# Kernel optimization log

Measured on AMD Instinct MI355X. Metric: run time of the kernel, lower is better.

Reference implementation:

```python
import jax, jax.numpy as jnp
import numpy as np

H1, H2 = 96, 64


def _lstm_scan(x_tbd, Wih, Whh, bih, bhh, hidden):
    """x_tbd: [T, B, D]. Returns (outputs [T, B, hidden], final h [B, hidden]).
    PyTorch gate order: i, f, g, o."""
    T, B, _ = x_tbd.shape
    b = bih + bhh  # fuse biases once
    # precompute input projections for all timesteps: [T, B, 4H]
    x_proj = jnp.einsum('tbd,hd->tbh', x_tbd, Wih) + b

    def step(carry, xp):
        h, c = carry
        gates = xp + h @ Whh.T  # [B, 4H]
        i, f, g, o = jnp.split(gates, 4, axis=-1)
        i = jax.nn.sigmoid(i)
        f = jax.nn.sigmoid(f)
        g = jnp.tanh(g)
        o = jax.nn.sigmoid(o)
        c = f * c + i * g
        h = o * jnp.tanh(c)
        return (h, c), h

    h0 = jnp.zeros((B, hidden), x_tbd.dtype)
    c0 = jnp.zeros((B, hidden), x_tbd.dtype)
    (hT, _), hs = jax.lax.scan(step, (h0, c0), x_proj)
    return hs, hT


def setup_inputs() -> dict:
    key = jax.random.key(0)
    ks = jax.random.split(key, 16)
    B, T, D, HOR = 4096, 336, 8, 24
    s1 = 1.0 / np.sqrt(H1)
    s2 = 1.0 / np.sqrt(H2)
    u = lambda k, shape, s: jax.random.uniform(k, shape, jnp.float32, -s, s)
    return {
        'x': jax.random.normal(ks[0], (B, T, D), jnp.float32),
        'Wih1': u(ks[1], (4 * H1, D), s1),
        'Whh1': u(ks[2], (4 * H1, H1), s1),
        'bih1': u(ks[3], (4 * H1,), s1),
        'bhh1': u(ks[4], (4 * H1,), s1),
        'Wih2': u(ks[5], (4 * H2, H1), s2),
        'Whh2': u(ks[6], (4 * H2, H2), s2),
        'bih2': u(ks[7], (4 * H2,), s2),
        'bhh2': u(ks[8], (4 * H2,), s2),
        'fc1_w': u(ks[9], (64, H2), s2),
        'fc1_b': u(ks[10], (64,), s2),
        'fco_w': u(ks[11], (HOR, 64), s2),
        'fco_b': u(ks[12], (HOR,), s2),
    }


def reference(x, Wih1, Whh1, bih1, bhh1, Wih2, Whh2, bih2, bhh2,
              fc1_w, fc1_b, fco_w, fco_b):
    # dropout layers are identity in eval mode
    x_tbd = jnp.transpose(x, (1, 0, 2))  # [T, B, D]
    hs1, _ = _lstm_scan(x_tbd, Wih1, Whh1, bih1, bhh1, H1)  # [T, B, 96]
    _, hT2 = _lstm_scan(hs1, Wih2, Whh2, bih2, bhh2, H2)    # [B, 64] = last timestep
    h = jax.nn.relu(hT2 @ fc1_w.T + fc1_b)
    return h @ fco_w.T + fco_b  # [B, horizon]
```

## Files before the change

kernel.cpp:

```cpp
#include <hip/hip_runtime.h>
#include <hip/hip_bf16.h>

namespace {

constexpr int T_LEN = 336;
constexpr int D_IN  = 8;
constexpr int NH1   = 96;
constexpr int NH2   = 64;
constexpr int HOR   = 24;
constexpr int BM    = 16;
constexpr int KPAD  = 200;


typedef __attribute__((ext_vector_type(8))) short short8;
typedef __attribute__((ext_vector_type(4))) float f32x4;

__device__ inline unsigned short f2b(float f) {
  union { float f; unsigned u; } v; v.f = f;
  unsigned r = v.u + 0x7fffu + ((v.u >> 16) & 1u);
  return (unsigned short)(r >> 16);
}

__device__ inline short8 pack8(float4 p0, float4 p1) {
  short8 f;
  f[0]=(short)f2b(p0.x); f[1]=(short)f2b(p0.y); f[2]=(short)f2b(p0.z); f[3]=(short)f2b(p0.w);
  f[4]=(short)f2b(p1.x); f[5]=(short)f2b(p1.y); f[6]=(short)f2b(p1.z); f[7]=(short)f2b(p1.w);
  return f;
}

__device__ inline float sigf(float x)   { return __builtin_amdgcn_rcpf(1.0f + __expf(-x)); }
__device__ inline float tanhf_(float x) { return 1.0f - 2.0f * __builtin_amdgcn_rcpf(1.0f + __expf(2.0f * x)); }

__global__ __launch_bounds__(512, 2) void lstm_forecaster(
    const float* __restrict__ x,
    const float* __restrict__ Wih1, const float* __restrict__ Whh1,
    const float* __restrict__ bih1, const float* __restrict__ bhh1,
    const float* __restrict__ Wih2, const float* __restrict__ Whh2,
    const float* __restrict__ bih2, const float* __restrict__ bhh2,
    const float* __restrict__ fc1w, const float* __restrict__ fc1b,
    const float* __restrict__ fcow, const float* __restrict__ fcob,
    float* __restrict__ out)
{
  __shared__ unsigned short Hc[2][BM * KPAD];
  __shared__ float h2f[BM][NH2];
  __shared__ float fcb[BM][NH2 + 4];

  const int tid  = threadIdx.x;
  const int w    = tid >> 6;
  const int l    = tid & 63;
  const int lrow = l & 15;
  const int lgrp = l >> 4;
  const int b0   = blockIdx.x * BM;

  const float* xrow = x + (size_t)(b0 + lrow) * (T_LEN * D_IN) + lgrp * 2;
  float2 xv = make_float2(0.0f, 0.0f);
  if (w == 0) xv = *(const float2*)(xrow);

  for (int i = tid; i < 2 * BM * KPAD; i += 512) ((unsigned short*)Hc)[i] = 0;

  short8 a1[3][4];
  #pragma unroll
  for (int mt = 0; mt < 3; ++mt) {
    const int gate = lrow & 3;
    const int cell = w * 12 + mt * 4 + (lrow >> 2);
    const int wrow = NH1 * gate + cell;
    #pragma unroll
    for (int kt = 0; kt < 4; ++kt) {
      const int kb = kt * 32 + lgrp * 8;
      if (kb < NH1) {
        a1[mt][kt] = pack8(*(const float4*)(Whh1 + wrow * NH1 + kb),
                           *(const float4*)(Whh1 + wrow * NH1 + kb + 4));
      } else if (kb == NH1) {
        a1[mt][kt] = pack8(*(const float4*)(Wih1 + wrow * D_IN),
                           *(const float4*)(Wih1 + wrow * D_IN + 4));
      } else {
        short8 z;
        #pragma unroll
        for (int e = 0; e < 8; ++e) z[e] = 0;
        a1[mt][kt] = z;
      }
    }
  }
  short8 a2[2][5];
  #pragma unroll
  for (int mt = 0; mt < 2; ++mt) {
    const int gate = lrow & 3;
    const int cell = w * 8 + mt * 4 + (lrow >> 2);
    const int wrow = NH2 * gate + cell;
    #pragma unroll
    for (int kt = 0; kt < 5; ++kt) {
      const int kb = kt * 32 + lgrp * 8;
      if (kb < NH2) {
        a2[mt][kt] = pack8(*(const float4*)(Whh2 + wrow * NH2 + kb),
                           *(const float4*)(Whh2 + wrow * NH2 + kb + 4));
      } else {
        a2[mt][kt] = pack8(*(const float4*)(Wih2 + wrow * NH1 + (kb - NH2)),
                           *(const float4*)(Wih2 + wrow * NH1 + (kb - NH2) + 4));
      }
    }
  }

  float bias1[3][4], bias2[2][4];
  #pragma unroll
  for (int mt = 0; mt < 3; ++mt) {
    const int cell = w * 12 + mt * 4 + lgrp;
    #pragma unroll
    for (int r = 0; r < 4; ++r)
      bias1[mt][r] = bih1[NH1 * r + cell] + bhh1[NH1 * r + cell];
  }
  #pragma unroll
  for (int mt = 0; mt < 2; ++mt) {
    const int cell = w * 8 + mt * 4 + lgrp;
    #pragma unroll
    for (int r = 0; r < 4; ++r)
      bias2[mt][r] = bih2[NH2 * r + cell] + bhh2[NH2 * r + cell];
  }

  __syncthreads();
  if (w == 0) {
    unsigned p = (unsigned)f2b(xv.x) | ((unsigned)f2b(xv.y) << 16);
    *(unsigned*)&Hc[1][lrow * KPAD + 160 + lgrp * 2] = p;
  }
  __syncthreads();

  float c1[3] = {0.0f, 0.0f, 0.0f};
  float c2[2] = {0.0f, 0.0f};
  const int rbo = lrow * KPAD;

  {
    if (w == 0) xv = *(const float2*)(xrow + D_IN);
    short8 b1[4];
    #pragma unroll
    for (int kt = 0; kt < 4; ++kt)
      b1[kt] = *(const short8*)(&Hc[1][rbo + 64 + lgrp * 8 + kt * 32]);
    #pragma unroll
    for (int mt = 0; mt < 3; ++mt) {
      f32x4 acc = { bias1[mt][0], bias1[mt][1], bias1[mt][2], bias1[mt][3] };
      #pragma unroll
      for (int kt = 0; kt < 4; ++kt)
        acc = __builtin_amdgcn_mfma_f32_16x16x32_bf16(a1[mt][kt], b1[kt], acc, 0, 0, 0);
      const float ig = sigf(acc[0]), fg = sigf(acc[1]);
      const float gg = tanhf_(acc[2]), og = sigf(acc[3]);
      c1[mt] = fg * c1[mt] + ig * gg;
      Hc[0][rbo + 64 + w * 12 + mt * 4 + lgrp] = f2b(og * tanhf_(c1[mt]));
    }
    if (w == 0) {
      unsigned p = (unsigned)f2b(xv.x) | ((unsigned)f2b(xv.y) << 16);
      *(unsigned*)&Hc[0][lrow * KPAD + 160 + lgrp * 2] = p;
    }
    __syncthreads();
  }

  for (int p = 0; p < T_LEN - 1; ++p) {
    const unsigned short* RB = &Hc[p & 1][0];
    unsigned short*       WB = &Hc[(p & 1) ^ 1][0];

    if (w == 0 && p + 2 < T_LEN)
      xv = *(const float2*)(xrow + (p + 2) * D_IN);

    short8 b2[5], b1[4];
    #pragma unroll
    for (int kt = 0; kt < 5; ++kt)
      b2[kt] = *(const short8*)(RB + rbo + lgrp * 8 + kt * 32);
    #pragma unroll
    for (int kt = 0; kt < 4; ++kt)
      b1[kt] = *(const short8*)(RB + rbo + 64 + lgrp * 8 + kt * 32);

    f32x4 acc2[2];
    #pragma unroll
    for (int mt = 0; mt < 2; ++mt) {
      acc2[mt] = f32x4{ bias2[mt][0], bias2[mt][1], bias2[mt][2], bias2[mt][3] };
      #pragma unroll
      for (int kt = 0; kt < 5; ++kt)
        acc2[mt] = __builtin_amdgcn_mfma_f32_16x16x32_bf16(a2[mt][kt], b2[kt], acc2[mt], 0, 0, 0);
    }
    f32x4 acc1[3];
    #pragma unroll
    for (int mt = 0; mt < 3; ++mt) {
      acc1[mt] = f32x4{ bias1[mt][0], bias1[mt][1], bias1[mt][2], bias1[mt][3] };
      #pragma unroll
      for (int kt = 0; kt < 4; ++kt)
        acc1[mt] = __builtin_amdgcn_mfma_f32_16x16x32_bf16(a1[mt][kt], b1[kt], acc1[mt], 0, 0, 0);
    }

    #pragma unroll
    for (int mt = 0; mt < 2; ++mt) {
      const float ig = sigf(acc2[mt][0]), fg = sigf(acc2[mt][1]);
      const float gg = tanhf_(acc2[mt][2]), og = sigf(acc2[mt][3]);
      c2[mt] = fg * c2[mt] + ig * gg;
      WB[rbo + w * 8 + mt * 4 + lgrp] = f2b(og * tanhf_(c2[mt]));
    }
    #pragma unroll
    for (int mt = 0; mt < 3; ++mt) {
      const float ig = sigf(acc1[mt][0]), fg = sigf(acc1[mt][1]);
      const float gg = tanhf_(acc1[mt][2]), og = sigf(acc1[mt][3]);
      c1[mt] = fg * c1[mt] + ig * gg;
      WB[rbo + 64 + w * 12 + mt * 4 + lgrp] = f2b(og * tanhf_(c1[mt]));
    }
    if (w == 0 && p + 2 < T_LEN) {
      unsigned pk = (unsigned)f2b(xv.x) | ((unsigned)f2b(xv.y) << 16);
      *(unsigned*)&WB[lrow * KPAD + 160 + lgrp * 2] = pk;
    }
    __syncthreads();
  }

  {
    const unsigned short* RB = &Hc[(T_LEN - 1) & 1][0];
    short8 b2[5];
    #pragma unroll
    for (int kt = 0; kt < 5; ++kt)
      b2[kt] = *(const short8*)(RB + rbo + lgrp * 8 + kt * 32);
    #pragma unroll
    for (int mt = 0; mt < 2; ++mt) {
      f32x4 acc = { bias2[mt][0], bias2[mt][1], bias2[mt][2], bias2[mt][3] };
      #pragma unroll
      for (int kt = 0; kt < 5; ++kt)
        acc = __builtin_amdgcn_mfma_f32_16x16x32_bf16(a2[mt][kt], b2[kt], acc, 0, 0, 0);
      const float ig = sigf(acc[0]), fg = sigf(acc[1]);
      const float gg = tanhf_(acc[2]), og = sigf(acc[3]);
      const float cf = fg * c2[mt] + ig * gg;
      h2f[lrow][w * 8 + mt * 4 + lgrp] = og * tanhf_(cf);
    }
  }
  __syncthreads();

  for (int p = tid; p < BM * NH2; p += 512) {
    const int col = p >> 6;
    const int j   = p & 63;
    float s = fc1b[j];
    const float* wr = fc1w + j * NH2;
    #pragma unroll 8
    for (int k = 0; k < NH2; ++k) s += h2f[col][k] * wr[k];
    fcb[col][j] = fmaxf(s, 0.0f);
  }
  __syncthreads();
  if (tid < BM * HOR) {
    const int col = tid / HOR;
    const int oc  = tid - col * HOR;
    float s = fcob[oc];
    const float* wr = fcow + oc * NH2;
    #pragma unroll 8
    for (int k = 0; k < NH2; ++k) s += fcb[col][k] * wr[k];
    out[(size_t)(b0 + col) * HOR + oc] = s;
  }
}

}

extern "C" void kernel_launch(void* const* d_in, const int* in_sizes, int n_in,
                              void* d_out, int out_size, void* d_ws, size_t ws_size,
                              hipStream_t stream) {
  const float* x    = (const float*)d_in[0];
  const float* Wih1 = (const float*)d_in[1];
  const float* Whh1 = (const float*)d_in[2];
  const float* bih1 = (const float*)d_in[3];
  const float* bhh1 = (const float*)d_in[4];
  const float* Wih2 = (const float*)d_in[5];
  const float* Whh2 = (const float*)d_in[6];
  const float* bih2 = (const float*)d_in[7];
  const float* bhh2 = (const float*)d_in[8];
  const float* fc1w = (const float*)d_in[9];
  const float* fc1b = (const float*)d_in[10];
  const float* fcow = (const float*)d_in[11];
  const float* fcob = (const float*)d_in[12];
  float* out = (float*)d_out;

  const int Btot = in_sizes[0] / (T_LEN * D_IN);
  const int nblk = Btot / BM;

  lstm_forecaster<<<dim3(nblk), dim3(512), 0, stream>>>(
      x, Wih1, Whh1, bih1, bhh1, Wih2, Whh2, bih2, bhh2,
      fc1w, fc1b, fcow, fcob, out);
}
```

Before: 361.6 us.

## Split layer-1 and layer-2 LSTM work across separate wave groups

The block grows from 512 to 1024 threads. Waves 0-7 now compute only layer 1 and waves 8-15 compute only layer 2, where before every wave computed both layers. Each wave holds about half as many weight fragments in registers, and the two layers' MFMA and activation chains run concurrently on different waves. Float-to-bf16 conversion also switches to the packed v_cvt_pk_bf16_f32 instruction. The risks are that the 1024-thread block with launch bounds of 4 blocks per CU squeezes the register budget, and that the per-step barrier now spans twice as many waves.

Measured after the change: 343.5 us. 5.0% less time.

```diff
diff --git a/kernel.cpp b/kernel.cpp
--- a/kernel.cpp
+++ b/kernel.cpp
@@ -28,10 +28,16 @@
   return f;
 }
 
+__device__ inline unsigned cvt_pk_bf16(float a, float b) {
+  unsigned r;
+  asm("v_cvt_pk_bf16_f32 %0, %1, %2" : "=v"(r) : "v"(a), "v"(b));
+  return r;
+}
+
 __device__ inline float sigf(float x)   { return __builtin_amdgcn_rcpf(1.0f + __expf(-x)); }
 __device__ inline float tanhf_(float x) { return 1.0f - 2.0f * __builtin_amdgcn_rcpf(1.0f + __expf(2.0f * x)); }
 
-__global__ __launch_bounds__(512, 2) void lstm_forecaster(
+__global__ __launch_bounds__(1024, 4) void lstm_forecaster(
     const float* __restrict__ x,
     const float* __restrict__ Wih1, const float* __restrict__ Whh1,
     const float* __restrict__ bih1, const float* __restrict__ bhh1,
@@ -51,102 +57,98 @@
   const int lrow = l & 15;
   const int lgrp = l >> 4;
   const int b0   = blockIdx.x * BM;
+  const bool isL1 = (w < 8);
+  const int  wv   = isL1 ? w : (w - 8);
 
   const float* xrow = x + (size_t)(b0 + lrow) * (T_LEN * D_IN) + lgrp * 2;
   float2 xv = make_float2(0.0f, 0.0f);
-  if (w == 0) xv = *(const float2*)(xrow);
-
-  for (int i = tid; i < 2 * BM * KPAD; i += 512) ((unsigned short*)Hc)[i] = 0;
-
-  short8 a1[3][4];
-  #pragma unroll
-  for (int mt = 0; mt < 3; ++mt) {
-    const int gate = lrow & 3;
-    const int cell = w * 12 + mt * 4 + (lrow >> 2);
-    const int wrow = NH1 * gate + cell;
-    #pragma unroll
-    for (int kt = 0; kt < 4; ++kt) {
-      const int kb = kt * 32 + lgrp * 8;
-      if (kb < NH1) {
-        a1[mt][kt] = pack8(*(const float4*)(Whh1 + wrow * NH1 + kb),
-                           *(const float4*)(Whh1 + wrow * NH1 + kb + 4));
-      } else if (kb == NH1) {
-        a1[mt][kt] = pack8(*(const float4*)(Wih1 + wrow * D_IN),
-                           *(const float4*)(Wih1 + wrow * D_IN + 4));
-      } else {
-        short8 z;
+  if (w == 8) xv = *(const float2*)(xrow);
+
+  for (int i = tid; i < 2 * BM * KPAD; i += 1024) ((unsigned short*)Hc)[i] = 0;
+
+  short8 af[12];
+  float  bs[12];
+  if (isL1) {
+    #pragma unroll
+    for (int mt = 0; mt < 3; ++mt) {
+      const int gate = lrow & 3;
+      const int cell = wv * 12 + mt * 4 + (lrow >> 2);
+      const int wrow = NH1 * gate + cell;
+      #pragma unroll
+      for (int kt = 0; kt < 4; ++kt) {
+        const int kb = kt * 32 + lgrp * 8;
+        if (kb < NH1) {
+          af[mt*4+kt] = pack8(*(const float4*)(Whh1 + wrow * NH1 + kb),
+                              *(const float4*)(Whh1 + wrow * NH1 + kb + 4));
+        } else if (kb == NH1) {
+          af[mt*4+kt] = pack8(*(const float4*)(Wih1 + wrow * D_IN),
+                              *(const float4*)(Wih1 + wrow * D_IN + 4));
+        } else {
+          short8 z;
+          #pragma unroll
+          for (int e = 0; e < 8; ++e) z[e] = 0;
+          af[mt*4+kt] = z;
+        }
+      }
+      const int bcell = wv * 12 + mt * 4 + lgrp;
+      #pragma unroll
+      for (int r = 0; r < 4; ++r)
+        bs[mt*4+r] = bih1[NH1 * r + bcell] + bhh1[NH1 * r + bcell];
+    }
+  } else {
+    #pragma unroll
+    for (int mt = 0; mt < 2; ++mt) {
+      const int gate = lrow & 3;
+      const int cell = wv * 8 + mt * 4 + (lrow >> 2);
+      const int wrow = NH2 * gate + cell;
+      #pragma unroll
+      for (int kt = 0; kt < 5; ++kt) {
+        const int kb = kt * 32 + lgrp * 8;
+        if (kb < NH2) {
+          af[mt*5+kt] = pack8(*(const float4*)(Whh2 + wrow * NH2 + kb),
+                              *(const float4*)(Whh2 + wrow * NH2 + kb + 4));
+        } else {
+          af[mt*5+kt] = pack8(*(const float4*)(Wih2 + wrow * NH1 + (kb - NH2)),
+                              *(const float4*)(Wih2 + wrow * NH1 + (kb - NH2) + 4));
+        }
+      }
+      const int bcell = wv * 8 + mt * 4 + lgrp;
+      #pragma unroll
+      for (int r = 0; r < 4; ++r)
+        bs[mt*4+r] = bih2[NH2 * r + bcell] + bhh2[NH2 * r + bcell];
+    }
+  }
+
+  __syncthreads();
+  if (w == 8) {
+    *(unsigned*)&Hc[1][lrow * KPAD + 160 + lgrp * 2] = cvt_pk_bf16(xv.x, xv.y);
+  }
+  __syncthreads();
+
+  float c[3] = {0.0f, 0.0f, 0.0f};
+  const int rbo = lrow * KPAD;
+
+  {
+    if (w == 8) {
+      xv = *(const float2*)(xrow + D_IN);
+      *(unsigned*)&Hc[0][rbo + 160 + lgrp * 2] = cvt_pk_bf16(xv.x, xv.y);
+    }
+    if (isL1) {
+      short8 bf[4];
+      #pragma unroll
+      for (int kt = 0; kt < 4; ++kt)
+        bf[kt] = *(const short8*)(&Hc[1][rbo + 64 + lgrp * 8 + kt * 32]);
+      #pragma unroll
+      for (int mt = 0; mt < 3; ++mt) {
+        f32x4 acc = { bs[mt*4+0], bs[mt*4+1], bs[mt*4+2], bs[mt*4+3] };
         #pragma unroll
-        for (int e = 0; e < 8; ++e) z[e] = 0;
-        a1[mt][kt] = z;
-      }
-    }
-  }
-  short8 a2[2][5];
-  #pragma unroll
-  for (int mt = 0; mt < 2; ++mt) {
-    const int gate = lrow & 3;
-    const int cell = w * 8 + mt * 4 + (lrow >> 2);
-    const int wrow = NH2 * gate + cell;
-    #pragma unroll
-    for (int kt = 0; kt < 5; ++kt) {
-      const int kb = kt * 32 + lgrp * 8;
-      if (kb < NH2) {
-        a2[mt][kt] = pack8(*(const float4*)(Whh2 + wrow * NH2 + kb),
-                           *(const float4*)(Whh2 + wrow * NH2 + kb + 4));
-      } else {
-        a2[mt][kt] = pack8(*(const float4*)(Wih2 + wrow * NH1 + (kb - NH2)),
-                           *(const float4*)(Wih2 + wrow * NH1 + (kb - NH2) + 4));
-      }
-    }
-  }
-
-  float bias1[3][4], bias2[2][4];
-  #pragma unroll
-  for (int mt = 0; mt < 3; ++mt) {
-    const int cell = w * 12 + mt * 4 + lgrp;
-    #pragma unroll
-    for (int r = 0; r < 4; ++r)
-      bias1[mt][r] = bih1[NH1 * r + cell] + bhh1[NH1 * r + cell];
-  }
-  #pragma unroll
-  for (int mt = 0; mt < 2; ++mt) {
-    const int cell = w * 8 + mt * 4 + lgrp;
-    #pragma unroll
-    for (int r = 0; r < 4; ++r)
-      bias2[mt][r] = bih2[NH2 * r + cell] + bhh2[NH2 * r + cell];
-  }
-
-  __syncthreads();
-  if (w == 0) {
-    unsigned p = (unsigned)f2b(xv.x) | ((unsigned)f2b(xv.y) << 16);
-    *(unsigned*)&Hc[1][lrow * KPAD + 160 + lgrp * 2] = p;
-  }
-  __syncthreads();
-
-  float c1[3] = {0.0f, 0.0f, 0.0f};
-  float c2[2] = {0.0f, 0.0f};
-  const int rbo = lrow * KPAD;
-
-  {
-    if (w == 0) xv = *(const float2*)(xrow + D_IN);
-    short8 b1[4];
-    #pragma unroll
-    for (int kt = 0; kt < 4; ++kt)
-      b1[kt] = *(const short8*)(&Hc[1][rbo + 64 + lgrp * 8 + kt * 32]);
-    #pragma unroll
-    for (int mt = 0; mt < 3; ++mt) {
-      f32x4 acc = { bias1[mt][0], bias1[mt][1], bias1[mt][2], bias1[mt][3] };
-      #pragma unroll
-      for (int kt = 0; kt < 4; ++kt)
-        acc = __builtin_amdgcn_mfma_f32_16x16x32_bf16(a1[mt][kt], b1[kt], acc, 0, 0, 0);
-      const float ig = sigf(acc[0]), fg = sigf(acc[1]);
-      const float gg = tanhf_(acc[2]), og = sigf(acc[3]);
-      c1[mt] = fg * c1[mt] + ig * gg;
-      Hc[0][rbo + 64 + w * 12 + mt * 4 + lgrp] = f2b(og * tanhf_(c1[mt]));
-    }
-    if (w == 0) {
-      unsigned p = (unsigned)f2b(xv.x) | ((unsigned)f2b(xv.y) << 16);
-      *(unsigned*)&Hc[0][lrow * KPAD + 160 + lgrp * 2] = p;
+        for (int kt = 0; kt < 4; ++kt)
+          acc = __builtin_amdgcn_mfma_f32_16x16x32_bf16(af[mt*4+kt], bf[kt], acc, 0, 0, 0);
+        const float ig = sigf(acc[0]), fg = sigf(acc[1]);
+        const float gg = tanhf_(acc[2]), og = sigf(acc[3]);
+        c[mt] = fg * c[mt] + ig * gg;
+        Hc[0][rbo + 64 + wv * 12 + mt * 4 + lgrp] = f2b(og * tanhf_(c[mt]));
+      }
     }
     __syncthreads();
   }
@@ -155,78 +157,79 @@
     const unsigned short* RB = &Hc[p & 1][0];
     unsigned short*       WB = &Hc[(p & 1) ^ 1][0];
 
-    if (w == 0 && p + 2 < T_LEN)
-      xv = *(const float2*)(xrow + (p + 2) * D_IN);
-
-    short8 b2[5], b1[4];
+    if (isL1) {
+      short8 bf[4];
+      #pragma unroll
+      for (int kt = 0; kt < 4; ++kt)
+        bf[kt] = *(const short8*)(RB + rbo + 64 + lgrp * 8 + kt * 32);
+      float h1v[3];
+      #pragma unroll
+      for (int mt = 0; mt < 3; ++mt) {
+        f32x4 acc = { bs[mt*4+0], bs[mt*4+1], bs[mt*4+2], bs[mt*4+3] };
+        #pragma unroll
+        for (int kt = 0; kt < 4; ++kt)
+          acc = __builtin_amdgcn_mfma_f32_16x16x32_bf16(af[mt*4+kt], bf[kt], acc, 0, 0, 0);
+        const float ig = sigf(acc[0]), fg = sigf(acc[1]);
+        const float gg = tanhf_(acc[2]), og = sigf(acc[3]);
+        c[mt] = fg * c[mt] + ig * gg;
+        h1v[mt] = og * tanhf_(c[mt]);
+      }
+      const unsigned pk01 = cvt_pk_bf16(h1v[0], h1v[1]);
+      const unsigned pk2  = cvt_pk_bf16(h1v[2], h1v[2]);
+      WB[rbo + 64 + wv * 12 + 0 + lgrp] = (unsigned short)pk01;
+      WB[rbo + 64 + wv * 12 + 4 + lgrp] = (unsigned short)(pk01 >> 16);
+      WB[rbo + 64 + wv * 12 + 8 + lgrp] = (unsigned short)pk2;
+    } else {
+      if (w == 8 && p + 2 < T_LEN)
+        xv = *(const float2*)(xrow + (p + 2) * D_IN);
+      short8 bf[5];
+      #pragma unroll
+      for (int kt = 0; kt < 5; ++kt)
+        bf[kt] = *(const short8*)(RB + rbo + lgrp * 8 + kt * 32);
+      float h2v[2];
+      #pragma unroll
+      for (int mt = 0; mt < 2; ++mt) {
+        f32x4 acc = { bs[mt*4+0], bs[mt*4+1], bs[mt*4+2], bs[mt*4+3] };
+        #pragma unroll
+        for (int kt = 0; kt < 5; ++kt)
+          acc = __builtin_amdgcn_mfma_f32_16x16x32_bf16(af[mt*5+kt], bf[kt], acc, 0, 0, 0);
+        const float ig = sigf(acc[0]), fg = sigf(acc[1]);
+        const float gg = tanhf_(acc[2]), og = sigf(acc[3]);
+        c[mt] = fg * c[mt] + ig * gg;
+        h2v[mt] = og * tanhf_(c[mt]);
+      }
+      const unsigned pk = cvt_pk_bf16(h2v[0], h2v[1]);
+      WB[rbo + wv * 8 + 0 + lgrp] = (unsigned short)pk;
+      WB[rbo + wv * 8 + 4 + lgrp] = (unsigned short)(pk >> 16);
+      if (w == 8 && p + 2 < T_LEN)
+        *(unsigned*)&WB[rbo + 160 + lgrp * 2] = cvt_pk_bf16(xv.x, xv.y);
+    }
+    __syncthreads();
+  }
+
+  if (!isL1) {
+    const unsigned short* RB = &Hc[(T_LEN - 1) & 1][0];
+    short8 bf[5];
     #pragma unroll
     for (int kt = 0; kt < 5; ++kt)
-      b2[kt] = *(const short8*)(RB + rbo + lgrp * 8 + kt * 32);
-    #pragma unroll
-    for (int kt = 0; kt < 4; ++kt)
-      b1[kt] = *(const short8*)(RB + rbo + 64 + lgrp * 8 + kt * 32);
-
-    f32x4 acc2[2];
+      bf[kt] = *(const short8*)(RB + rbo + lgrp * 8 + kt * 32);
     #pragma unroll
     for (int mt = 0; mt < 2; ++mt) {
-      acc2[mt] = f32x4{ bias2[mt][0], bias2[mt][1], bias2[mt][2], bias2[mt][3] };
+      f32x4 acc = { bs[mt*4+0], bs[mt*4+1], bs[mt*4+2], bs[mt*4+3] };
       #pragma unroll
       for (int kt = 0; kt < 5; ++kt)
-        acc2[mt] = __builtin_amdgcn_mfma_f32_16x16x32_bf16(a2[mt][kt], b2[kt], acc2[mt], 0, 0, 0);
-    }
-    f32x4 acc1[3];
-    #pragma unroll
-    for (int mt = 0; mt < 3; ++mt) {
-      acc1[mt] = f32x4{ bias1[mt][0], bias1[mt][1], bias1[mt][2], bias1[mt][3] };
-      #pragma unroll
-      for (int kt = 0; kt < 4; ++kt)
-        acc1[mt] = __builtin_amdgcn_mfma_f32_16x16x32_bf16(a1[mt][kt], b1[kt], acc1[mt], 0, 0, 0);
-    }
-
-    #pragma unroll
-    for (int mt = 0; mt < 2; ++mt) {
-      const float ig = sigf(acc2[mt][0]), fg = sigf(acc2[mt][1]);
-      const float gg = tanhf_(acc2[mt][2]), og = sigf(acc2[mt][3]);
-      c2[mt] = fg * c2[mt] + ig * gg;
-      WB[rbo + w * 8 + mt * 4 + lgrp] = f2b(og * tanhf_(c2[mt]));
-    }
-    #pragma unroll
-    for (int mt = 0; mt < 3; ++mt) {
-      const float ig = sigf(acc1[mt][0]), fg = sigf(acc1[mt][1]);
-      const float gg = tanhf_(acc1[mt][2]), og = sigf(acc1[mt][3]);
-      c1[mt] = fg * c1[mt] + ig * gg;
-      WB[rbo + 64 + w * 12 + mt * 4 + lgrp] = f2b(og * tanhf_(c1[mt]));
-    }
-    if (w == 0 && p + 2 < T_LEN) {
-      unsigned pk = (unsigned)f2b(xv.x) | ((unsigned)f2b(xv.y) << 16);
-      *(unsigned*)&WB[lrow * KPAD + 160 + lgrp * 2] = pk;
-    }
-    __syncthreads();
-  }
-
-  {
-    const unsigned short* RB = &Hc[(T_LEN - 1) & 1][0];
-    short8 b2[5];
-    #pragma unroll
-    for (int kt = 0; kt < 5; ++kt)
-      b2[kt] = *(const short8*)(RB + rbo + lgrp * 8 + kt * 32);
-    #pragma unroll
-    for (int mt = 0; mt < 2; ++mt) {
-      f32x4 acc = { bias2[mt][0], bias2[mt][1], bias2[mt][2], bias2[mt][3] };
-      #pragma unroll
-      for (int kt = 0; kt < 5; ++kt)
-        acc = __builtin_amdgcn_mfma_f32_16x16x32_bf16(a2[mt][kt], b2[kt], acc, 0, 0, 0);
+        acc = __builtin_amdgcn_mfma_f32_16x16x32_bf16(af[mt*5+kt], bf[kt], acc, 0, 0, 0);
       const float ig = sigf(acc[0]), fg = sigf(acc[1]);
       const float gg = tanhf_(acc[2]), og = sigf(acc[3]);
-      const float cf = fg * c2[mt] + ig * gg;
-      h2f[lrow][w * 8 + mt * 4 + lgrp] = og * tanhf_(cf);
-    }
-  }
-  __syncthreads();
-
-  for (int p = tid; p < BM * NH2; p += 512) {
-    const int col = p >> 6;
-    const int j   = p & 63;
+      const float cf = fg * c[mt] + ig * gg;
+      h2f[lrow][wv * 8 + mt * 4 + lgrp] = og * tanhf_(cf);
+    }
+  }
+  __syncthreads();
+
+  {
+    const int col = tid >> 6;
+    const int j   = tid & 63;
     float s = fc1b[j];
     const float* wr = fc1w + j * NH2;
     #pragma unroll 8
@@ -268,7 +271,7 @@
   const int Btot = in_sizes[0] / (T_LEN * D_IN);
   const int nblk = Btot / BM;
 
-  lstm_forecaster<<<dim3(nblk), dim3(512), 0, stream>>>(
+  lstm_forecaster<<<dim3(nblk), dim3(1024), 0, stream>>>(
       x, Wih1, Whh1, bih1, bhh1, Wih2, Whh2, bih2, bhh2,
       fc1w, fc1b, fcow, fcob, out);
 }
```
